# Kernel tuning notes

Measured on AMD Instinct MI355X. Metric: run time of the kernel, lower is better.

## Reference

```python
import jax, jax.numpy as jnp
import numpy as np

BN_EPS = 1e-5


def setup_inputs() -> dict:
    key = jax.random.key(0)
    ks = jax.random.split(key, 6)
    N, F, H, C, E = 50000, 128, 256, 40, 800000
    x = jax.random.normal(ks[0], (N, F), dtype=jnp.float32)
    edge_index = jax.random.randint(ks[1], (2, E), 0, N, dtype=jnp.int64)
    eps = jnp.zeros((), dtype=jnp.float32)  # train_eps=True, init 0
    W1 = jax.random.normal(ks[2], (F, H), dtype=jnp.float32) * (1.0 / np.sqrt(F))
    b1 = jnp.zeros((H,), dtype=jnp.float32)
    gamma = jnp.ones((H,), dtype=jnp.float32)
    beta = jnp.zeros((H,), dtype=jnp.float32)
    W2 = jax.random.normal(ks[3], (H, C), dtype=jnp.float32) * (1.0 / np.sqrt(H))
    b2 = jnp.zeros((C,), dtype=jnp.float32)
    return {"x": x, "edge_index": edge_index, "eps": eps, "W1": W1, "b1": b1,
            "gamma": gamma, "beta": beta, "W2": W2, "b2": b2}


def reference(x, edge_index, eps, W1, b1, gamma, beta, W2, b2):
    N = x.shape[0]
    src, dst = edge_index[0], edge_index[1]  # source_to_target flow
    # GIN sum aggregation: sum_{j in N(i)} x_j  (scatter-add over edges)
    agg = jax.ops.segment_sum(x[src], dst, num_segments=N)
    h = (1.0 + eps) * x + agg  # [N, F]
    # MLP: Linear -> ReLU (act_first) -> BatchNorm -> Linear (plain last)
    h = jax.nn.relu(h @ W1 + b1)  # [N, H]
    mean = jnp.mean(h, axis=0)
    var = jnp.var(h, axis=0)  # biased var, training-mode batch norm
    h = (h - mean) * jax.lax.rsqrt(var + BN_EPS) * gamma + beta
    out = h @ W2 + b2  # [N, C]
    return jax.nn.log_softmax(out, axis=-1)
```

## Files before the change

### kernel.cpp

```cpp
#include <hip/hip_runtime.h>
#include <hip/hip_bf16.h>
#include <math.h>

#define F_IN 128
#define H_DIM 256
#define C_OUT 40

typedef __attribute__((ext_vector_type(8))) short short8v;
typedef __attribute__((ext_vector_type(4))) float float4v;

__device__ __forceinline__ unsigned short f2bf(float f) {
    union { float f; unsigned int u; } c; c.f = f;
    unsigned int r = (c.u + 0x7fffu + ((c.u >> 16) & 1u)) >> 16;
    return (unsigned short)r;
}
__device__ __forceinline__ float bf2f(unsigned short u) {
    union { unsigned int u; float f; } c; c.u = ((unsigned int)u) << 16;
    return c.f;
}

__global__ __launch_bounds__(256) void prep(const float* __restrict__ x,
                                            const float* __restrict__ W1,
                                            const int* __restrict__ src,
                                            const int* __restrict__ dst,
                                            unsigned short* __restrict__ x_b,
                                            unsigned short* __restrict__ w1t,
                                            int* __restrict__ head,
                                            int2* __restrict__ listbuf,
                                            int N, int E, int nA) {
    int b = blockIdx.x;
    if (b < nA) {
        long long i = ((long long)b * 256 + threadIdx.x) * 8;
        if (i + 7 < (long long)N * F_IN) {
            float4 v0 = *reinterpret_cast<const float4*>(x + i);
            float4 v1 = *reinterpret_cast<const float4*>(x + i + 4);
            short8v o;
            o[0] = (short)f2bf(v0.x); o[1] = (short)f2bf(v0.y);
            o[2] = (short)f2bf(v0.z); o[3] = (short)f2bf(v0.w);
            o[4] = (short)f2bf(v1.x); o[5] = (short)f2bf(v1.y);
            o[6] = (short)f2bf(v1.z); o[7] = (short)f2bf(v1.w);
            *reinterpret_cast<short8v*>(x_b + i) = o;
        }
    } else if (b < nA + 128) {
        int t = (b - nA) * 2 + (threadIdx.x >> 7);
        int k = threadIdx.x & 127;
        w1t[t * F_IN + k] = f2bf(W1[(size_t)k * H_DIM + t]);
    } else {
        int i = (b - nA - 128) * 256 + threadIdx.x;
        if (i < E) {
            int d = dst[i];
            int prev = atomicExch(&head[d], i + 1);
            listbuf[i] = make_int2(src[i], prev);
        }
    }
}

__global__ __launch_bounds__(256) void gather_agg(const unsigned short* __restrict__ xb,
                                                  const float* __restrict__ epsp,
                                                  const int* __restrict__ head,
                                                  const int2* __restrict__ listbuf,
                                                  unsigned short* __restrict__ aggb, int N) {
    int wave = (blockIdx.x * 256 + (int)threadIdx.x) >> 6;
    int lane = threadIdx.x & 63;
    int g = lane >> 3;
    int lr = lane & 7;
    int node = wave * 8 + g;
    bool valid = node < N;
    int j = valid ? head[node] : 0;

    float acc[16] = {};
    while (__any(j > 0)) {
        if (j > 0) {
            int2 e = listbuf[j - 1];
            const unsigned short* rp = xb + (size_t)e.x * F_IN + lr * 16;
            short8v v0 = *reinterpret_cast<const short8v*>(rp);
            short8v v1 = *reinterpret_cast<const short8v*>(rp + 8);
            j = e.y;
            #pragma unroll
            for (int t = 0; t < 8; ++t) acc[t] += bf2f((unsigned short)v0[t]);
            #pragma unroll
            for (int t = 0; t < 8; ++t) acc[8 + t] += bf2f((unsigned short)v1[t]);
        }
    }

    if (valid) {
        float sc = 1.0f + epsp[0];
        const unsigned short* xp = xb + (size_t)node * F_IN + lr * 16;
        short8v x0 = *reinterpret_cast<const short8v*>(xp);
        short8v x1 = *reinterpret_cast<const short8v*>(xp + 8);
        short8v o0, o1;
        #pragma unroll
        for (int t = 0; t < 8; ++t) {
            o0[t] = (short)f2bf(fmaf(sc, bf2f((unsigned short)x0[t]), acc[t]));
            o1[t] = (short)f2bf(fmaf(sc, bf2f((unsigned short)x1[t]), acc[8 + t]));
        }
        unsigned short* op = aggb + (size_t)node * F_IN + lr * 16;
        *reinterpret_cast<short8v*>(op) = o0;
        *reinterpret_cast<short8v*>(op + 8) = o1;
    }
}

__global__ __launch_bounds__(256) void gemm1_mfma(const unsigned short* __restrict__ agg_b,
                                                  const unsigned short* __restrict__ w1t,
                                                  const float* __restrict__ b1,
                                                  unsigned short* __restrict__ h1,
                                                  float* __restrict__ partials, int N) {
    __shared__ short As[128][136];
    __shared__ short Bs[128][136];
    __shared__ float sums_l[128], ssq_l[128];

    int tid = threadIdx.x;
    int m0 = blockIdx.x * 128;
    int n0 = blockIdx.y * 128;

    if (tid < 128) { sums_l[tid] = 0.f; ssq_l[tid] = 0.f; }

    #pragma unroll
    for (int i = 0; i < 8; ++i) {
        int c = tid + i * 256;
        int row = c >> 4, ck = c & 15;
        int gr = m0 + row;
        short8v v = {0, 0, 0, 0, 0, 0, 0, 0};
        if (gr < N) v = *reinterpret_cast<const short8v*>(agg_b + (size_t)gr * F_IN + ck * 8);
        *reinterpret_cast<short8v*>(&As[row][ck * 8]) = v;
    }
    #pragma unroll
    for (int i = 0; i < 8; ++i) {
        int c = tid + i * 256;
        int row = c >> 4, ck = c & 15;
        *reinterpret_cast<short8v*>(&Bs[row][ck * 8]) =
            *reinterpret_cast<const short8v*>(w1t + (size_t)(n0 + row) * F_IN + ck * 8);
    }
    __syncthreads();

    int w = tid >> 6, lane = tid & 63;
    int wm = w >> 1, wn = w & 1;
    int lr = lane & 15, lk = (lane >> 4) * 8;

    float4v acc[4][4] = {};
    #pragma unroll
    for (int ks = 0; ks < 4; ++ks) {
        int k0 = ks * 32 + lk;
        short8v a[4], b[4];
        #pragma unroll
        for (int am = 0; am < 4; ++am)
            a[am] = *reinterpret_cast<short8v*>(&As[wm * 64 + am * 16 + lr][k0]);
        #pragma unroll
        for (int bn = 0; bn < 4; ++bn)
            b[bn] = *reinterpret_cast<short8v*>(&Bs[wn * 64 + bn * 16 + lr][k0]);
        #pragma unroll
        for (int am = 0; am < 4; ++am)
            #pragma unroll
            for (int bn = 0; bn < 4; ++bn)
                acc[am][bn] = __builtin_amdgcn_mfma_f32_16x16x32_bf16(a[am], b[bn], acc[am][bn], 0, 0, 0);
    }

    __syncthreads();
    short (*T)[136] = As;
    #pragma unroll
    for (int bn = 0; bn < 4; ++bn) {
        int col = wn * 64 + bn * 16 + lr;
        float bias = b1[n0 + col];
        float ps = 0.f, pss = 0.f;
        #pragma unroll
        for (int am = 0; am < 4; ++am) {
            #pragma unroll
            for (int r = 0; r < 4; ++r) {
                int rowl = wm * 64 + am * 16 + (lane >> 4) * 4 + r;
                float v = fmaxf(acc[am][bn][r] + bias, 0.f);
                unsigned short ub = f2bf(v);
                T[rowl][col] = (short)ub;
                if (m0 + rowl < N) {
                    float vr = bf2f(ub);
                    ps += vr;
                    pss = fmaf(vr, vr, pss);
                }
            }
        }
        atomicAdd(&sums_l[col], ps);
        atomicAdd(&ssq_l[col], pss);
    }
    __syncthreads();

    #pragma unroll
    for (int i = 0; i < 8; ++i) {
        int c = tid + i * 256;
        int row = c >> 4, ck = c & 15;
        int gr = m0 + row;
        if (gr < N)
            *reinterpret_cast<short8v*>(h1 + (size_t)gr * H_DIM + n0 + ck * 8) =
                *reinterpret_cast<short8v*>(&T[row][ck * 8]);
    }
    if (tid < 128) {
        size_t base = (size_t)blockIdx.x * 512;
        partials[base + n0 + tid] = sums_l[tid];
        partials[base + 256 + n0 + tid] = ssq_l[tid];
    }
}

__global__ __launch_bounds__(256) void bn_reduce(const float* __restrict__ partials,
                                                 int nbx,
                                                 float* __restrict__ sums,
                                                 float* __restrict__ sumsq) {
    __shared__ float red[8];
    int k = blockIdx.x;
    float s = 0.f, ss = 0.f;
    for (int b = threadIdx.x; b < nbx; b += 256) {
        s += partials[(size_t)b * 512 + k];
        ss += partials[(size_t)b * 512 + 256 + k];
    }
    #pragma unroll
    for (int off = 32; off > 0; off >>= 1) {
        s += __shfl_down(s, off, 64);
        ss += __shfl_down(ss, off, 64);
    }
    int wave = threadIdx.x >> 6;
    int lane = threadIdx.x & 63;
    if (lane == 0) { red[wave] = s; red[4 + wave] = ss; }
    __syncthreads();
    if (threadIdx.x == 0) {
        sums[k] = red[0] + red[1] + red[2] + red[3];
        sumsq[k] = red[4] + red[5] + red[6] + red[7];
    }
}

__global__ __launch_bounds__(256) void bn_fold(const float* __restrict__ sums,
                                               const float* __restrict__ sumsq,
                                               const float* __restrict__ gamma,
                                               const float* __restrict__ beta,
                                               const float* __restrict__ W2,
                                               const float* __restrict__ b2,
                                               unsigned short* __restrict__ w2frag,
                                               float* __restrict__ b2f, int N) {
    __shared__ float scale_s[H_DIM], shift_s[H_DIM];
    int k = threadIdx.x;
    float invN = 1.0f / (float)N;
    float mean = sums[k] * invN;
    float var = sumsq[k] * invN - mean * mean;
    float scale = gamma[k] * rsqrtf(var + 1e-5f);
    float shift = beta[k] - mean * scale;
    scale_s[k] = scale;
    shift_s[k] = shift;
    __syncthreads();
    if (k < 48) {
        if (k < C_OUT) {
            float acc = b2[k];
            for (int j = 0; j < H_DIM; ++j) acc = fmaf(shift_s[j], W2[j * C_OUT + k], acc);
            b2f[k] = acc;
        } else {
            b2f[k] = -1e30f;
        }
    }
    for (int u = threadIdx.x; u < 1536; u += 256) {
        int lane = u & 63, t = u >> 6;
        int ks = t / 3, bf = t - ks * 3;
        int col = bf * 16 + (lane & 15);
        int kb = ks * 32 + (lane >> 4) * 8;
        short8v o;
        #pragma unroll
        for (int e = 0; e < 8; ++e) {
            int kk = kb + e;
            float v = (col < C_OUT) ? scale_s[kk] * W2[kk * C_OUT + col] : 0.f;
            o[e] = (short)f2bf(v);
        }
        *reinterpret_cast<short8v*>(w2frag + (size_t)u * 8) = o;
    }
}

__global__ __launch_bounds__(256) void gemm2_lsm(const unsigned short* __restrict__ h1,
                                                 const unsigned short* __restrict__ w2frag,
                                                 const float* __restrict__ b2f,
                                                 float* __restrict__ out, int N) {
    int tid = threadIdx.x;
    int wm = tid >> 6;
    int lane = tid & 63;
    int lr = lane & 15;
    int g = lane >> 4;
    int row0 = blockIdx.x * 64 + wm * 16;
    int arow = row0 + lr;
    if (arow >= N) arow = N - 1;

    short8v a[8];
    const unsigned short* ap = h1 + (size_t)arow * H_DIM + g * 8;
    #pragma unroll
    for (int ks = 0; ks < 8; ++ks)
        a[ks] = *reinterpret_cast<const short8v*>(ap + ks * 32);

    float4v acc[3] = {};
    #pragma unroll
    for (int ks = 0; ks < 8; ++ks) {
        #pragma unroll
        for (int bf = 0; bf < 3; ++bf) {
            short8v b = *reinterpret_cast<const short8v*>(
                w2frag + (size_t)(((ks * 3 + bf) << 6) + lane) * 8);
            acc[bf] = __builtin_amdgcn_mfma_f32_16x16x32_bf16(a[ks], b, acc[bf], 0, 0, 0);
        }
    }

    float b0 = b2f[lr], b1v = b2f[16 + lr], b2v = b2f[32 + lr];
    #pragma unroll
    for (int r = 0; r < 4; ++r) {
        float v0 = acc[0][r] + b0;
        float v1 = acc[1][r] + b1v;
        float v2 = acc[2][r] + b2v;
        float m = fmaxf(fmaxf(v0, v1), v2);
        #pragma unroll
        for (int o = 1; o < 16; o <<= 1) m = fmaxf(m, __shfl_xor(m, o, 64));
        float s = __expf(v0 - m) + __expf(v1 - m) + __expf(v2 - m);
        #pragma unroll
        for (int o = 1; o < 16; o <<= 1) s += __shfl_xor(s, o, 64);
        float lse = m + __logf(s);
        int row = row0 + g * 4 + r;
        if (row < N) {
            float* op = out + (size_t)row * C_OUT;
            op[lr] = v0 - lse;
            op[16 + lr] = v1 - lse;
            if (lr < 8) op[32 + lr] = v2 - lse;
        }
    }
}

extern "C" void kernel_launch(void* const* d_in, const int* in_sizes, int n_in,
                              void* d_out, int out_size, void* d_ws, size_t ws_size,
                              hipStream_t stream) {
    const float* x     = (const float*)d_in[0];
    const int*   ei    = (const int*)d_in[1];
    const float* eps   = (const float*)d_in[2];
    const float* W1    = (const float*)d_in[3];
    const float* b1    = (const float*)d_in[4];
    const float* gamma = (const float*)d_in[5];
    const float* beta  = (const float*)d_in[6];
    const float* W2    = (const float*)d_in[7];
    const float* b2    = (const float*)d_in[8];
    float* out = (float*)d_out;

    int N = in_sizes[0] / F_IN;
    int E = in_sizes[1] / 2;
    const int* srcIdx = ei;
    const int* dstIdx = ei + E;

    int nbx = (N + 127) / 128;

    unsigned short* x_b    = (unsigned short*)d_ws;
    unsigned short* agg_b  = x_b + (size_t)N * F_IN;
    unsigned short* w1t    = agg_b + (size_t)N * F_IN;
    unsigned short* h1     = w1t + H_DIM * F_IN;
    float* partials = (float*)(h1 + (size_t)N * H_DIM);
    float* sums   = partials + (size_t)nbx * 512;
    float* sumsq  = sums + H_DIM;
    unsigned short* w2frag = (unsigned short*)(sumsq + H_DIM);
    float* b2f    = (float*)(w2frag + 1536 * 8);

    int*  head    = (int*)h1;
    int2* listbuf = (int2*)(head + N);

    hipMemsetAsync(head, 0, (size_t)N * sizeof(int), stream);

    int nA = (N * 16 + 255) / 256;
    int nE = (E + 255) / 256;
    hipLaunchKernelGGL(prep, dim3(nA + 128 + nE), dim3(256), 0, stream,
                       x, W1, srcIdx, dstIdx, x_b, w1t, head, listbuf, N, E, nA);

    hipLaunchKernelGGL(gather_agg, dim3((N + 31) / 32), dim3(256), 0, stream,
                       x_b, eps, head, listbuf, agg_b, N);

    dim3 g1(nbx, 2);
    hipLaunchKernelGGL(gemm1_mfma, g1, dim3(256), 0, stream,
                       agg_b, w1t, b1, h1, partials, N);

    hipLaunchKernelGGL(bn_reduce, dim3(H_DIM), dim3(256), 0, stream,
                       partials, nbx, sums, sumsq);

    hipLaunchKernelGGL(bn_fold, dim3(1), dim3(H_DIM), 0, stream,
                       sums, sumsq, gamma, beta, W2, b2, w2frag, b2f, N);

    hipLaunchKernelGGL(gemm2_lsm, dim3((N + 63) / 64), dim3(256), 0, stream,
                       h1, w2frag, b2f, out, N);
}
```

Baseline: 161.5 us.

## Split per-node edge lists in two chains and gather with two lane groups

Each destination node now keeps two linked lists, picked by edge-index parity, so the gather kernel can walk them with two 8-lane groups per node and combine the partial sums with a cross-lane shuffle. This halves the serial pointer-chasing depth per node and lowers contention on the head atomics. In exchange it launches twice as many waves, and list building moves out of the prep kernel into its own launch, which adds a launch and loses the overlap with the bf16 conversion of x.

```diff
diff --git a/kernel.cpp b/kernel.cpp
--- a/kernel.cpp
+++ b/kernel.cpp
@@ -21,13 +21,9 @@
 
 __global__ __launch_bounds__(256) void prep(const float* __restrict__ x,
                                             const float* __restrict__ W1,
-                                            const int* __restrict__ src,
-                                            const int* __restrict__ dst,
                                             unsigned short* __restrict__ x_b,
                                             unsigned short* __restrict__ w1t,
-                                            int* __restrict__ head,
-                                            int2* __restrict__ listbuf,
-                                            int N, int E, int nA) {
+                                            int N, int nA) {
     int b = blockIdx.x;
     if (b < nA) {
         long long i = ((long long)b * 256 + threadIdx.x) * 8;
@@ -41,18 +37,22 @@
             o[6] = (short)f2bf(v1.z); o[7] = (short)f2bf(v1.w);
             *reinterpret_cast<short8v*>(x_b + i) = o;
         }
-    } else if (b < nA + 128) {
+    } else {
         int t = (b - nA) * 2 + (threadIdx.x >> 7);
         int k = threadIdx.x & 127;
         w1t[t * F_IN + k] = f2bf(W1[(size_t)k * H_DIM + t]);
-    } else {
-        int i = (b - nA - 128) * 256 + threadIdx.x;
-        if (i < E) {
-            int d = dst[i];
-            int prev = atomicExch(&head[d], i + 1);
-            listbuf[i] = make_int2(src[i], prev);
-        }
-    }
+    }
+}
+
+__global__ __launch_bounds__(256) void build_list(const int* __restrict__ src,
+                                                  const int* __restrict__ dst,
+                                                  int* __restrict__ head,
+                                                  int2* __restrict__ listbuf, int E) {
+    int i = blockIdx.x * 256 + threadIdx.x;
+    if (i >= E) return;
+    int d = dst[i];
+    int prev = atomicExch(&head[d * 2 + (i & 1)], i + 1);
+    listbuf[i] = make_int2(src[i], prev);
 }
 
 __global__ __launch_bounds__(256) void gather_agg(const unsigned short* __restrict__ xb,
@@ -62,11 +62,12 @@
                                                   unsigned short* __restrict__ aggb, int N) {
     int wave = (blockIdx.x * 256 + (int)threadIdx.x) >> 6;
     int lane = threadIdx.x & 63;
-    int g = lane >> 3;
+    int g = lane >> 4;
+    int c = (lane >> 3) & 1;
     int lr = lane & 7;
-    int node = wave * 8 + g;
+    int node = wave * 4 + g;
     bool valid = node < N;
-    int j = valid ? head[node] : 0;
+    int j = valid ? head[node * 2 + c] : 0;
 
     float acc[16] = {};
     while (__any(j > 0)) {
@@ -83,7 +84,10 @@
         }
     }
 
-    if (valid) {
+    #pragma unroll
+    for (int t = 0; t < 16; ++t) acc[t] += __shfl_xor(acc[t], 8, 64);
+
+    if (valid && c == 0) {
         float sc = 1.0f + epsp[0];
         const unsigned short* xp = xb + (size_t)node * F_IN + lr * 16;
         short8v x0 = *reinterpret_cast<const short8v*>(xp);
@@ -352,16 +356,18 @@
     float* b2f    = (float*)(w2frag + 1536 * 8);
 
     int*  head    = (int*)h1;
-    int2* listbuf = (int2*)(head + N);
-
-    hipMemsetAsync(head, 0, (size_t)N * sizeof(int), stream);
+    int2* listbuf = (int2*)(head + 2 * N);
+
+    hipMemsetAsync(head, 0, (size_t)2 * N * sizeof(int), stream);
 
     int nA = (N * 16 + 255) / 256;
-    int nE = (E + 255) / 256;
-    hipLaunchKernelGGL(prep, dim3(nA + 128 + nE), dim3(256), 0, stream,
-                       x, W1, srcIdx, dstIdx, x_b, w1t, head, listbuf, N, E, nA);
-
-    hipLaunchKernelGGL(gather_agg, dim3((N + 31) / 32), dim3(256), 0, stream,
+    hipLaunchKernelGGL(prep, dim3(nA + 128), dim3(256), 0, stream,
+                       x, W1, x_b, w1t, N, nA);
+
+    hipLaunchKernelGGL(build_list, dim3((E + 255) / 256), dim3(256), 0, stream,
+                       srcIdx, dstIdx, head, listbuf, E);
+
+    hipLaunchKernelGGL(gather_agg, dim3((N + 15) / 16), dim3(256), 0, stream,
                        x_b, eps, head, listbuf, agg_b, N);
 
     dim3 g1(nbx, 2);
```

After: 152.5 us. 5.6% less time.

## Fuse BN reduce and fold via last-block counter, split edge list build

Applied to the files above, without the earlier changes.

Merges the bn_reduce and bn_fold kernels into a single kernel. The last block to finish, found with an atomic counter, computes scale and shift and builds the folded W2 fragments, which removes one kernel launch. The edge linked-list construction also moves out of the prep kernel into its own build_list kernel. That split adds a launch back, but it keeps the atomic list work from sharing blocks with the x conversion. The counter reset is done inside prep, and the fused kernel relies on a threadfence plus relaxed atomics for correct ordering.

```diff
diff --git a/kernel.cpp b/kernel.cpp
--- a/kernel.cpp
+++ b/kernel.cpp
@@ -21,13 +21,10 @@
 
 __global__ __launch_bounds__(256) void prep(const float* __restrict__ x,
                                             const float* __restrict__ W1,
-                                            const int* __restrict__ src,
-                                            const int* __restrict__ dst,
                                             unsigned short* __restrict__ x_b,
                                             unsigned short* __restrict__ w1t,
-                                            int* __restrict__ head,
-                                            int2* __restrict__ listbuf,
-                                            int N, int E, int nA) {
+                                            int* __restrict__ bn_counter,
+                                            int N, int nA) {
     int b = blockIdx.x;
     if (b < nA) {
         long long i = ((long long)b * 256 + threadIdx.x) * 8;
@@ -41,18 +38,23 @@
             o[6] = (short)f2bf(v1.z); o[7] = (short)f2bf(v1.w);
             *reinterpret_cast<short8v*>(x_b + i) = o;
         }
-    } else if (b < nA + 128) {
+    } else {
+        if (b == nA && threadIdx.x == 0) *bn_counter = 0;
         int t = (b - nA) * 2 + (threadIdx.x >> 7);
         int k = threadIdx.x & 127;
         w1t[t * F_IN + k] = f2bf(W1[(size_t)k * H_DIM + t]);
-    } else {
-        int i = (b - nA - 128) * 256 + threadIdx.x;
-        if (i < E) {
-            int d = dst[i];
-            int prev = atomicExch(&head[d], i + 1);
-            listbuf[i] = make_int2(src[i], prev);
-        }
-    }
+    }
+}
+
+__global__ __launch_bounds__(256) void build_list(const int* __restrict__ src,
+                                                  const int* __restrict__ dst,
+                                                  int* __restrict__ head,
+                                                  int2* __restrict__ listbuf, int E) {
+    int i = blockIdx.x * 256 + threadIdx.x;
+    if (i >= E) return;
+    int d = dst[i];
+    int prev = atomicExch(&head[d], i + 1);
+    listbuf[i] = make_int2(src[i], prev);
 }
 
 __global__ __launch_bounds__(256) void gather_agg(const unsigned short* __restrict__ xb,
@@ -198,11 +200,20 @@
     }
 }
 
-__global__ __launch_bounds__(256) void bn_reduce(const float* __restrict__ partials,
-                                                 int nbx,
-                                                 float* __restrict__ sums,
-                                                 float* __restrict__ sumsq) {
+__global__ __launch_bounds__(256) void bn_reduce_fold(const float* __restrict__ partials,
+                                                      int nbx,
+                                                      float* __restrict__ sums,
+                                                      float* __restrict__ sumsq,
+                                                      int* __restrict__ counter,
+                                                      const float* __restrict__ gamma,
+                                                      const float* __restrict__ beta,
+                                                      const float* __restrict__ W2,
+                                                      const float* __restrict__ b2,
+                                                      unsigned short* __restrict__ w2frag,
+                                                      float* __restrict__ b2f, int N) {
     __shared__ float red[8];
+    __shared__ int s_last;
+    __shared__ float scale_s[H_DIM], shift_s[H_DIM];
     int k = blockIdx.x;
     float s = 0.f, ss = 0.f;
     for (int b = threadIdx.x; b < nbx; b += 256) {
@@ -219,43 +230,42 @@
     if (lane == 0) { red[wave] = s; red[4 + wave] = ss; }
     __syncthreads();
     if (threadIdx.x == 0) {
-        sums[k] = red[0] + red[1] + red[2] + red[3];
-        sumsq[k] = red[4] + red[5] + red[6] + red[7];
-    }
-}
-
-__global__ __launch_bounds__(256) void bn_fold(const float* __restrict__ sums,
-                                               const float* __restrict__ sumsq,
-                                               const float* __restrict__ gamma,
-                                               const float* __restrict__ beta,
-                                               const float* __restrict__ W2,
-                                               const float* __restrict__ b2,
-                                               unsigned short* __restrict__ w2frag,
-                                               float* __restrict__ b2f, int N) {
-    __shared__ float scale_s[H_DIM], shift_s[H_DIM];
-    int k = threadIdx.x;
+        float st = red[0] + red[1] + red[2] + red[3];
+        float sst = red[4] + red[5] + red[6] + red[7];
+        __hip_atomic_store(&sums[k], st, __ATOMIC_RELAXED, __HIP_MEMORY_SCOPE_AGENT);
+        __hip_atomic_store(&sumsq[k], sst, __ATOMIC_RELAXED, __HIP_MEMORY_SCOPE_AGENT);
+        __threadfence();
+        int old = atomicAdd(counter, 1);
+        s_last = (old == (int)gridDim.x - 1) ? 1 : 0;
+    }
+    __syncthreads();
+    if (!s_last) return;
+
+    int t = threadIdx.x;
+    float sv = __hip_atomic_load(&sums[t], __ATOMIC_RELAXED, __HIP_MEMORY_SCOPE_AGENT);
+    float ssv = __hip_atomic_load(&sumsq[t], __ATOMIC_RELAXED, __HIP_MEMORY_SCOPE_AGENT);
     float invN = 1.0f / (float)N;
-    float mean = sums[k] * invN;
-    float var = sumsq[k] * invN - mean * mean;
-    float scale = gamma[k] * rsqrtf(var + 1e-5f);
-    float shift = beta[k] - mean * scale;
-    scale_s[k] = scale;
-    shift_s[k] = shift;
-    __syncthreads();
-    if (k < 48) {
-        if (k < C_OUT) {
-            float acc = b2[k];
-            for (int j = 0; j < H_DIM; ++j) acc = fmaf(shift_s[j], W2[j * C_OUT + k], acc);
-            b2f[k] = acc;
+    float mean = sv * invN;
+    float var = ssv * invN - mean * mean;
+    float scale = gamma[t] * rsqrtf(var + 1e-5f);
+    float shift = beta[t] - mean * scale;
+    scale_s[t] = scale;
+    shift_s[t] = shift;
+    __syncthreads();
+    if (t < 48) {
+        if (t < C_OUT) {
+            float acc = b2[t];
+            for (int j = 0; j < H_DIM; ++j) acc = fmaf(shift_s[j], W2[j * C_OUT + t], acc);
+            b2f[t] = acc;
         } else {
-            b2f[k] = -1e30f;
-        }
-    }
-    for (int u = threadIdx.x; u < 1536; u += 256) {
-        int lane = u & 63, t = u >> 6;
-        int ks = t / 3, bf = t - ks * 3;
-        int col = bf * 16 + (lane & 15);
-        int kb = ks * 32 + (lane >> 4) * 8;
+            b2f[t] = -1e30f;
+        }
+    }
+    for (int u = t; u < 1536; u += 256) {
+        int lane2 = u & 63, tt = u >> 6;
+        int ks = tt / 3, bf = tt - ks * 3;
+        int col = bf * 16 + (lane2 & 15);
+        int kb = ks * 32 + (lane2 >> 4) * 8;
         short8v o;
         #pragma unroll
         for (int e = 0; e < 8; ++e) {
@@ -348,7 +358,8 @@
     float* partials = (float*)(h1 + (size_t)N * H_DIM);
     float* sums   = partials + (size_t)nbx * 512;
     float* sumsq  = sums + H_DIM;
-    unsigned short* w2frag = (unsigned short*)(sumsq + H_DIM);
+    int*   bn_ctr = (int*)(sumsq + H_DIM);
+    unsigned short* w2frag = (unsigned short*)(bn_ctr + 8);
     float* b2f    = (float*)(w2frag + 1536 * 8);
 
     int*  head    = (int*)h1;
@@ -357,9 +368,11 @@
     hipMemsetAsync(head, 0, (size_t)N * sizeof(int), stream);
 
     int nA = (N * 16 + 255) / 256;
-    int nE = (E + 255) / 256;
-    hipLaunchKernelGGL(prep, dim3(nA + 128 + nE), dim3(256), 0, stream,
-                       x, W1, srcIdx, dstIdx, x_b, w1t, head, listbuf, N, E, nA);
+    hipLaunchKernelGGL(prep, dim3(nA + 128), dim3(256), 0, stream,
+                       x, W1, x_b, w1t, bn_ctr, N, nA);
+
+    hipLaunchKernelGGL(build_list, dim3((E + 255) / 256), dim3(256), 0, stream,
+                       srcIdx, dstIdx, head, listbuf, E);
 
     hipLaunchKernelGGL(gather_agg, dim3((N + 31) / 32), dim3(256), 0, stream,
                        x_b, eps, head, listbuf, agg_b, N);
@@ -368,11 +381,9 @@
     hipLaunchKernelGGL(gemm1_mfma, g1, dim3(256), 0, stream,
                        agg_b, w1t, b1, h1, partials, N);
 
-    hipLaunchKernelGGL(bn_reduce, dim3(H_DIM), dim3(256), 0, stream,
-                       partials, nbx, sums, sumsq);
-
-    hipLaunchKernelGGL(bn_fold, dim3(1), dim3(H_DIM), 0, stream,
-                       sums, sumsq, gamma, beta, W2, b2, w2frag, b2f, N);
+    hipLaunchKernelGGL(bn_reduce_fold, dim3(H_DIM), dim3(256), 0, stream,
+                       partials, nbx, sums, sumsq, bn_ctr,
+                       gamma, beta, W2, b2, w2frag, b2f, N);
 
     hipLaunchKernelGGL(gemm2_lsm, dim3((N + 63) / 64), dim3(256), 0, stream,
                        h1, w2frag, b2f, out, N);
```

Measured after the change: 155.8 us. -3.5%, faster.
